# Kernel tuning notes

Measured on AMD Instinct MI355X. Metric: run time of the kernel, lower is better.

## Reference

```python
import jax, jax.numpy as jnp
import numpy as np

TEMP = 50.0  # softmax temperature from __init__ (temp=50.0)

N_SAMPLES = 32768
NUM_CANDIDATES = 2048
NUM_DIMS = 16


def setup_inputs() -> dict:
    key = jax.random.key(0)
    k1, k2, k3 = jax.random.split(key, 3)
    X = jax.random.normal(k1, (N_SAMPLES, NUM_DIMS), dtype=jnp.float32)
    Y = jax.random.normal(k2, (1, NUM_CANDIDATES, NUM_DIMS), dtype=jnp.float32)  # Y_rest param
    b = jax.random.normal(k3, (1, NUM_CANDIDATES), dtype=jnp.float32) * 0.1     # intercept_rest param
    return {"X": X, "Y": Y, "b": b}


def reference(X, Y, b):
    """FiniteModel.forward in convex mode with soft selection.

    scores[n, c] = <X[n], Y[0, c]> - b[0, c]           (dot-product kernel)
    weights      = softmax(temp * scores, axis=1)       (moded_max, soft mode)
    f_x[n]       = sum_c weights[n, c] * scores[n, c]
    choice[n, :] = sum_c weights[n, c] * Y[0, c, :]
    Returns (choice, f_x) as in the torch forward.
    """
    Yc = Y[0]                                     # [C, D]
    scores = jnp.einsum('nd,cd->nc', X, Yc) - b   # [N, C] (b broadcasts from [1, C])
    weights = jax.nn.softmax(TEMP * scores, axis=1)
    f_x = jnp.sum(weights * scores, axis=1)       # [N]
    choice = jnp.einsum('nc,cd->nd', weights, Yc) # [N, D]
    return choice, f_x
```

## Files before the change

kernel.cpp:

```cpp
#include <hip/hip_runtime.h>
#include <math.h>

#if defined(__has_builtin)
#  if __has_builtin(__builtin_amdgcn_exp2f)
#    define EXP2F(x) __builtin_amdgcn_exp2f(x)
#  else
#    define EXP2F(x) exp2f(x)
#  endif
#else
#  define EXP2F(x) exp2f(x)
#endif

constexpr int   DD = 16;
constexpr float T2 = 72.13475204444817f;
constexpr float DEFER_THR = 8.0f;

typedef __attribute__((ext_vector_type(8)))  short s16x8;
typedef __attribute__((ext_vector_type(16))) float f32x16;

static __device__ __forceinline__ s16x8 mk8(unsigned a, unsigned b, unsigned c, unsigned d) {
    union { unsigned u[4]; s16x8 v; } x;
    x.u[0] = a; x.u[1] = b; x.u[2] = c; x.u[3] = d;
    return x.v;
}
static __device__ __forceinline__ unsigned pack_tr(float a, float b) {
    return (__float_as_uint(a) >> 16) | (__float_as_uint(b) & 0xFFFF0000u);
}
static __device__ __forceinline__ float trunc_bf(float a) {
    return __uint_as_float(__float_as_uint(a) & 0xFFFF0000u);
}
static __device__ __forceinline__ unsigned short rne16(float f) {
    unsigned u = __float_as_uint(f);
    return (unsigned short)((u + 0x7FFFu + ((u >> 16) & 1u)) >> 16);
}
static __device__ __forceinline__ float bfh2f(unsigned short h) {
    return __uint_as_float(((unsigned)h) << 16);
}

__global__ void prep_kernel(const float* __restrict__ Y, const float* __restrict__ B,
                            unsigned short* __restrict__ YhA, unsigned short* __restrict__ YlA,
                            unsigned short* __restrict__ V3h, unsigned short* __restrict__ V3l,
                            unsigned* __restrict__ Bq, int C)
{
    int c = blockIdx.x * blockDim.x + threadIdx.x;
    if (c >= C) return;

    union { unsigned short u[DD]; s16x8 v[2]; } hb, lb;
    const float* yr = Y + (size_t)c * DD;
#pragma unroll
    for (int d = 0; d < DD; ++d) {
        float y = yr[d];
        unsigned short h = rne16(y);
        hb.u[d] = h;
        lb.u[d] = rne16(y - bfh2f(h));
    }
    s16x8* yh = (s16x8*)(YhA + (size_t)c * DD);
    s16x8* yl = (s16x8*)(YlA + (size_t)c * DD);
    yh[0] = hb.v[0]; yh[1] = hb.v[1];
    yl[0] = lb.v[0]; yl[1] = lb.v[1];

    float bb = B[c];
    float qb = -T2 * bb;
    unsigned short qh = rne16(qb);
    Bq[c] = (unsigned)qh | ((unsigned)rne16(qb - bfh2f(qh)) << 16);

    const int t = c >> 5, r = c & 31;
    union { unsigned short u[32]; s16x8 v[4]; } vh, vl;
#pragma unroll
    for (int slot = 0; slot < 32; ++slot) {
        int j = slot & 7, hs = (slot >> 3) & 1;
        int cl = (slot & 16) | (j & 3) | (hs << 2) | (((j >> 2) & 1) << 3);
        int cc = (t << 5) | cl;
        float v;
        if (r < DD)            v = Y[(size_t)cc * DD + r];
        else if (r == DD)      v = B[cc];
        else if (r == DD + 1)  v = 1.0f;
        else                   v = 0.0f;
        unsigned short h = rne16(v);
        vh.u[slot] = h;
        vl.u[slot] = rne16(v - bfh2f(h));
    }
    s16x8* ph = (s16x8*)(V3h + ((size_t)t * 32 + r) * 32);
    s16x8* pl = (s16x8*)(V3l + ((size_t)t * 32 + r) * 32);
#pragma unroll
    for (int q = 0; q < 4; ++q) { ph[q] = vh.v[q]; pl[q] = vl.v[q]; }
}

struct Frag {
    s16x8 aYh, aYl, vh0, vh1, vl0, vl1;
    unsigned bw;
};

__global__ __launch_bounds__(256, 4)
void finite_mfma(const float* __restrict__ X,
                 const unsigned short* __restrict__ YhA, const unsigned short* __restrict__ YlA,
                 const unsigned short* __restrict__ V3h, const unsigned short* __restrict__ V3l,
                 const unsigned* __restrict__ Bq,
                 float* __restrict__ out, int N, int C)
{
    const int tid  = threadIdx.x;
    const int wave = tid >> 6, lane = tid & 63;
    const int s = lane & 31, hi = lane >> 5;
    const int n0 = blockIdx.x * 32;
    const int cpw = C >> 2, cbase = wave * cpw, ntile = cpw >> 5;

    __shared__ float bufc[4][18][32];
    __shared__ float lds_m[4][32];

    const unsigned short* pYh = YhA + ((size_t)(cbase + s) * DD + 8 * hi);
    const unsigned short* pYl = YlA + ((size_t)(cbase + s) * DD + 8 * hi);
    const unsigned short* pVh = V3h + (((size_t)(cbase >> 5) * 32 + s) * 32 + 8 * hi);
    const unsigned short* pVl = V3l + (((size_t)(cbase >> 5) * 32 + s) * 32 + 8 * hi);
    const unsigned*       pBq = Bq + cbase + s;

    const float* xp = X + ((size_t)(n0 + s) * DD + 8 * hi);
    float xq[8];
#pragma unroll
    for (int jj = 0; jj < 8; ++jj) xq[jj] = xp[jj] * T2;
    unsigned xhw[4], xlw[4];
#pragma unroll
    for (int jj = 0; jj < 4; ++jj) {
        float a = xq[2 * jj], b = xq[2 * jj + 1];
        xhw[jj] = pack_tr(a, b);
        xlw[jj] = pack_tr(a - trunc_bf(a), b - trunc_bf(b));
    }
    const s16x8 xqh = mk8(xhw[0], xhw[1], xhw[2], xhw[3]);
    const s16x8 xql = mk8(xlw[0], xlw[1], xlw[2], xlw[3]);
    const s16x8 ones2 = mk8(hi ? 0u : 0x3F803F80u, 0u, 0u, 0u);

    f32x16 acc;
#pragma unroll
    for (int r = 0; r < 16; ++r) acc[r] = 0.0f;
    float m2 = -INFINITY;

#define LDF(F, k) do {                                              \
        (F).aYh = *(const s16x8*)(pYh + (size_t)(k) * 512);         \
        (F).aYl = *(const s16x8*)(pYl + (size_t)(k) * 512);         \
        (F).vh0 = *(const s16x8*)(pVh + (size_t)(k) * 1024);        \
        (F).vh1 = *(const s16x8*)(pVh + (size_t)(k) * 1024 + 16);   \
        (F).vl0 = *(const s16x8*)(pVl + (size_t)(k) * 1024);        \
        (F).vl1 = *(const s16x8*)(pVl + (size_t)(k) * 1024 + 16);   \
        (F).bw  = pBq[(size_t)(k) * 32];                            \
    } while (0)

#define PROC(F) do {                                                            \
        const s16x8 a2 = mk8(hi ? 0u : (F).bw, 0u, 0u, 0u);                     \
        f32x16 S;                                                               \
        _Pragma("unroll")                                                       \
        for (int r = 0; r < 16; ++r) S[r] = 0.0f;                               \
        S = __builtin_amdgcn_mfma_f32_32x32x16_bf16(a2,     ones2, S, 0, 0, 0); \
        S = __builtin_amdgcn_mfma_f32_32x32x16_bf16((F).aYh, xqh,  S, 0, 0, 0); \
        S = __builtin_amdgcn_mfma_f32_32x32x16_bf16((F).aYh, xql,  S, 0, 0, 0); \
        S = __builtin_amdgcn_mfma_f32_32x32x16_bf16((F).aYl, xqh,  S, 0, 0, 0); \
        float tm[8];                                                            \
        _Pragma("unroll")                                                       \
        for (int jj = 0; jj < 8; ++jj) tm[jj] = fmaxf(S[2 * jj], S[2 * jj + 1]);\
        _Pragma("unroll")                                                       \
        for (int jj = 0; jj < 4; ++jj) tm[jj] = fmaxf(tm[jj], tm[jj + 4]);      \
        tm[0] = fmaxf(fmaxf(tm[0], tm[2]), fmaxf(tm[1], tm[3]));                \
        float tmax = fmaxf(tm[0], __shfl_xor(tm[0], 32, 64));                   \
        if (__any(tmax > m2 + DEFER_THR)) {                                     \
            float nm = fmaxf(m2, tmax);                                         \
            float sc = EXP2F(m2 - nm);                                          \
            _Pragma("unroll")                                                   \
            for (int r = 0; r < 16; ++r) acc[r] *= sc;                          \
            m2 = nm;                                                            \
        }                                                                       \
        unsigned phw[8];                                                        \
        _Pragma("unroll")                                                       \
        for (int jj = 0; jj < 8; ++jj) {                                        \
            float e0 = EXP2F(S[2 * jj] - m2);                                   \
            float e1 = EXP2F(S[2 * jj + 1] - m2);                               \
            phw[jj] = pack_tr(e0, e1);                                          \
        }                                                                       \
        const s16x8 Bph0 = mk8(phw[0], phw[1], phw[2], phw[3]);                 \
        const s16x8 Bph1 = mk8(phw[4], phw[5], phw[6], phw[7]);                 \
        acc = __builtin_amdgcn_mfma_f32_32x32x16_bf16((F).vh0, Bph0, acc, 0, 0, 0); \
        acc = __builtin_amdgcn_mfma_f32_32x32x16_bf16((F).vl0, Bph0, acc, 0, 0, 0); \
        acc = __builtin_amdgcn_mfma_f32_32x32x16_bf16((F).vh1, Bph1, acc, 0, 0, 0); \
        acc = __builtin_amdgcn_mfma_f32_32x32x16_bf16((F).vl1, Bph1, acc, 0, 0, 0); \
    } while (0)

    Frag f0, f1;
    LDF(f0, 0);
    for (int t = 0; t < ntile; t += 2) {
        LDF(f1, t + 1);
        PROC(f0);
        if (t + 2 < ntile) LDF(f0, t + 2);
        PROC(f1);
    }
#undef LDF
#undef PROC

    if (hi == 0) lds_m[wave][s] = m2;
    __syncthreads();
    float mstar = fmaxf(fmaxf(lds_m[0][s], lds_m[1][s]), fmaxf(lds_m[2][s], lds_m[3][s]));
    float sw = EXP2F(m2 - mstar);
#pragma unroll
    for (int r = 0; r < 8; ++r) {
        int dv = (r & 3) + 8 * (r >> 2) + 4 * hi;
        bufc[wave][dv][s] = acc[r] * sw;
    }
    if (hi == 0) {
        bufc[wave][16][s] = acc[8] * sw;
        bufc[wave][17][s] = acc[9] * sw;
    }
    __syncthreads();

#pragma unroll
    for (int q = 0; q < 3; ++q) {
        int u = tid + 256 * q;
        if (u < 18 * 32) {
            int dv = u >> 5, ss = u & 31;
            bufc[0][dv][ss] = bufc[0][dv][ss] + bufc[1][dv][ss]
                            + bufc[2][dv][ss] + bufc[3][dv][ss];
        }
    }
    __syncthreads();

    {
        int ss = tid >> 3, d0 = (tid & 7) * 2;
        float inv = 1.0f / bufc[0][17][ss];
        float2 o = make_float2(bufc[0][d0][ss] * inv, bufc[0][d0 + 1][ss] * inv);
        *(float2*)(out + (size_t)(n0 + ss) * DD + d0) = o;
    }
    if (tid < 32) {
        float inv = 1.0f / bufc[0][17][tid];
        const float* xr = X + (size_t)(n0 + tid) * DD;
        float dot = 0.0f;
#pragma unroll
        for (int d = 0; d < DD; ++d) dot = fmaf(xr[d], bufc[0][d][tid], dot);
        out[(size_t)N * DD + n0 + tid] = (dot - bufc[0][16][tid]) * inv;
    }
}

extern "C" void kernel_launch(void* const* d_in, const int* in_sizes, int n_in,
                              void* d_out, int out_size, void* d_ws, size_t ws_size,
                              hipStream_t stream) {
    const float* X = (const float*)d_in[0];
    const float* Y = (const float*)d_in[1];
    const float* B = (const float*)d_in[2];
    float*     out = (float*)d_out;

    const int N = in_sizes[0] / DD;
    const int C = in_sizes[2];

    char* w = (char*)d_ws;
    unsigned short* YhA = (unsigned short*)(w);
    unsigned short* YlA = (unsigned short*)(w + (size_t)C * DD * 2);
    unsigned short* V3h = (unsigned short*)(w + (size_t)C * DD * 4);
    unsigned short* V3l = (unsigned short*)(w + (size_t)C * DD * 4 + (size_t)32 * C * 2);
    unsigned*       Bq  = (unsigned*)   (w + (size_t)C * DD * 4 + (size_t)32 * C * 4);

    hipLaunchKernelGGL(prep_kernel, dim3((C + 255) / 256), dim3(256), 0, stream,
                       Y, B, YhA, YlA, V3h, V3l, Bq, C);
    hipLaunchKernelGGL(finite_mfma, dim3(N / 32), dim3(256), 0, stream,
                       X, YhA, YlA, V3h, V3l, Bq, out, N, C);
}
```

Baseline: 86.74 us.

## Drop low-bf16 V operand, widen blocks to eight waves, parallelize prep

Removes the low-order bf16 split of the value matrix, which halves the accumulation MFMAs and the V loads per tile. Raises the block size to 512 threads so eight waves split the candidates, with wider LDS reduction buffers to match. The prep kernel now gives each V element its own thread instead of looping 32 slots per candidate. Dropping the low split lowers the precision of the weighted sums of Y and b, and the accumulation now relies on single-bf16 values.

```diff
diff --git a/kernel.cpp b/kernel.cpp
--- a/kernel.cpp
+++ b/kernel.cpp
@@ -39,78 +39,66 @@
 
 __global__ void prep_kernel(const float* __restrict__ Y, const float* __restrict__ B,
                             unsigned short* __restrict__ YhA, unsigned short* __restrict__ YlA,
-                            unsigned short* __restrict__ V3h, unsigned short* __restrict__ V3l,
-                            unsigned* __restrict__ Bq, int C)
+                            unsigned short* __restrict__ V3h, unsigned* __restrict__ Bq, int C)
 {
-    int c = blockIdx.x * blockDim.x + threadIdx.x;
-    if (c >= C) return;
-
-    union { unsigned short u[DD]; s16x8 v[2]; } hb, lb;
-    const float* yr = Y + (size_t)c * DD;
-#pragma unroll
-    for (int d = 0; d < DD; ++d) {
-        float y = yr[d];
-        unsigned short h = rne16(y);
-        hb.u[d] = h;
-        lb.u[d] = rne16(y - bfh2f(h));
-    }
-    s16x8* yh = (s16x8*)(YhA + (size_t)c * DD);
-    s16x8* yl = (s16x8*)(YlA + (size_t)c * DD);
-    yh[0] = hb.v[0]; yh[1] = hb.v[1];
-    yl[0] = lb.v[0]; yl[1] = lb.v[1];
-
-    float bb = B[c];
-    float qb = -T2 * bb;
-    unsigned short qh = rne16(qb);
-    Bq[c] = (unsigned)qh | ((unsigned)rne16(qb - bfh2f(qh)) << 16);
-
-    const int t = c >> 5, r = c & 31;
-    union { unsigned short u[32]; s16x8 v[4]; } vh, vl;
-#pragma unroll
-    for (int slot = 0; slot < 32; ++slot) {
+    int gid = blockIdx.x * blockDim.x + threadIdx.x;
+    if (gid < C) {
+        const int c = gid;
+        union { unsigned short u[DD]; s16x8 v[2]; } hb, lb;
+        const float* yr = Y + (size_t)c * DD;
+#pragma unroll
+        for (int d = 0; d < DD; ++d) {
+            float y = yr[d];
+            unsigned short h = rne16(y);
+            hb.u[d] = h;
+            lb.u[d] = rne16(y - bfh2f(h));
+        }
+        s16x8* yh = (s16x8*)(YhA + (size_t)c * DD);
+        s16x8* yl = (s16x8*)(YlA + (size_t)c * DD);
+        yh[0] = hb.v[0]; yh[1] = hb.v[1];
+        yl[0] = lb.v[0]; yl[1] = lb.v[1];
+
+        float qb = -T2 * B[c];
+        unsigned short qh = rne16(qb);
+        Bq[c] = (unsigned)qh | ((unsigned)rne16(qb - bfh2f(qh)) << 16);
+    } else if (gid < C + 32 * C) {
+        const int e = gid - C;
+        const int t = e >> 10, r = (e >> 5) & 31, slot = e & 31;
         int j = slot & 7, hs = (slot >> 3) & 1;
         int cl = (slot & 16) | (j & 3) | (hs << 2) | (((j >> 2) & 1) << 3);
         int cc = (t << 5) | cl;
         float v;
-        if (r < DD)            v = Y[(size_t)cc * DD + r];
-        else if (r == DD)      v = B[cc];
-        else if (r == DD + 1)  v = 1.0f;
-        else                   v = 0.0f;
-        unsigned short h = rne16(v);
-        vh.u[slot] = h;
-        vl.u[slot] = rne16(v - bfh2f(h));
-    }
-    s16x8* ph = (s16x8*)(V3h + ((size_t)t * 32 + r) * 32);
-    s16x8* pl = (s16x8*)(V3l + ((size_t)t * 32 + r) * 32);
-#pragma unroll
-    for (int q = 0; q < 4; ++q) { ph[q] = vh.v[q]; pl[q] = vl.v[q]; }
+        if (r < DD)           v = Y[(size_t)cc * DD + r];
+        else if (r == DD)     v = B[cc];
+        else if (r == DD + 1) v = 1.0f;
+        else                  v = 0.0f;
+        V3h[((size_t)t * 32 + r) * 32 + slot] = rne16(v);
+    }
 }
 
 struct Frag {
-    s16x8 aYh, aYl, vh0, vh1, vl0, vl1;
+    s16x8 aYh, aYl, vh0, vh1;
     unsigned bw;
 };
 
-__global__ __launch_bounds__(256, 4)
+__global__ __launch_bounds__(512, 8)
 void finite_mfma(const float* __restrict__ X,
                  const unsigned short* __restrict__ YhA, const unsigned short* __restrict__ YlA,
-                 const unsigned short* __restrict__ V3h, const unsigned short* __restrict__ V3l,
-                 const unsigned* __restrict__ Bq,
+                 const unsigned short* __restrict__ V3h, const unsigned* __restrict__ Bq,
                  float* __restrict__ out, int N, int C)
 {
     const int tid  = threadIdx.x;
     const int wave = tid >> 6, lane = tid & 63;
     const int s = lane & 31, hi = lane >> 5;
     const int n0 = blockIdx.x * 32;
-    const int cpw = C >> 2, cbase = wave * cpw, ntile = cpw >> 5;
-
-    __shared__ float bufc[4][18][32];
-    __shared__ float lds_m[4][32];
+    const int cpw = C >> 3, cbase = wave * cpw, ntile = cpw >> 5;
+
+    __shared__ float bufc[8][18][32];
+    __shared__ float lds_m[8][32];
 
     const unsigned short* pYh = YhA + ((size_t)(cbase + s) * DD + 8 * hi);
     const unsigned short* pYl = YlA + ((size_t)(cbase + s) * DD + 8 * hi);
     const unsigned short* pVh = V3h + (((size_t)(cbase >> 5) * 32 + s) * 32 + 8 * hi);
-    const unsigned short* pVl = V3l + (((size_t)(cbase >> 5) * 32 + s) * 32 + 8 * hi);
     const unsigned*       pBq = Bq + cbase + s;
 
     const float* xp = X + ((size_t)(n0 + s) * DD + 8 * hi);
@@ -138,8 +126,6 @@
         (F).aYl = *(const s16x8*)(pYl + (size_t)(k) * 512);         \
         (F).vh0 = *(const s16x8*)(pVh + (size_t)(k) * 1024);        \
         (F).vh1 = *(const s16x8*)(pVh + (size_t)(k) * 1024 + 16);   \
-        (F).vl0 = *(const s16x8*)(pVl + (size_t)(k) * 1024);        \
-        (F).vl1 = *(const s16x8*)(pVl + (size_t)(k) * 1024 + 16);   \
         (F).bw  = pBq[(size_t)(k) * 32];                            \
     } while (0)
 
@@ -176,9 +162,7 @@
         const s16x8 Bph0 = mk8(phw[0], phw[1], phw[2], phw[3]);                 \
         const s16x8 Bph1 = mk8(phw[4], phw[5], phw[6], phw[7]);                 \
         acc = __builtin_amdgcn_mfma_f32_32x32x16_bf16((F).vh0, Bph0, acc, 0, 0, 0); \
-        acc = __builtin_amdgcn_mfma_f32_32x32x16_bf16((F).vl0, Bph0, acc, 0, 0, 0); \
         acc = __builtin_amdgcn_mfma_f32_32x32x16_bf16((F).vh1, Bph1, acc, 0, 0, 0); \
-        acc = __builtin_amdgcn_mfma_f32_32x32x16_bf16((F).vl1, Bph1, acc, 0, 0, 0); \
     } while (0)
 
     Frag f0, f1;
@@ -194,7 +178,9 @@
 
     if (hi == 0) lds_m[wave][s] = m2;
     __syncthreads();
-    float mstar = fmaxf(fmaxf(lds_m[0][s], lds_m[1][s]), fmaxf(lds_m[2][s], lds_m[3][s]));
+    float mstar = lds_m[0][s];
+#pragma unroll
+    for (int w = 1; w < 8; ++w) mstar = fmaxf(mstar, lds_m[w][s]);
     float sw = EXP2F(m2 - mstar);
 #pragma unroll
     for (int r = 0; r < 8; ++r) {
@@ -208,21 +194,22 @@
     __syncthreads();
 
 #pragma unroll
-    for (int q = 0; q < 3; ++q) {
-        int u = tid + 256 * q;
+    for (int q = 0; q < 2; ++q) {
+        int u = tid + 512 * q;
         if (u < 18 * 32) {
             int dv = u >> 5, ss = u & 31;
-            bufc[0][dv][ss] = bufc[0][dv][ss] + bufc[1][dv][ss]
-                            + bufc[2][dv][ss] + bufc[3][dv][ss];
+            float sum = bufc[0][dv][ss];
+#pragma unroll
+            for (int w = 1; w < 8; ++w) sum += bufc[w][dv][ss];
+            bufc[0][dv][ss] = sum;
         }
     }
     __syncthreads();
 
     {
-        int ss = tid >> 3, d0 = (tid & 7) * 2;
+        int ss = tid >> 4, d0 = tid & 15;
         float inv = 1.0f / bufc[0][17][ss];
-        float2 o = make_float2(bufc[0][d0][ss] * inv, bufc[0][d0 + 1][ss] * inv);
-        *(float2*)(out + (size_t)(n0 + ss) * DD + d0) = o;
+        out[(size_t)(n0 + ss) * DD + d0] = bufc[0][d0][ss] * inv;
     }
     if (tid < 32) {
         float inv = 1.0f / bufc[0][17][tid];
@@ -249,11 +236,11 @@
     unsigned short* YhA = (unsigned short*)(w);
     unsigned short* YlA = (unsigned short*)(w + (size_t)C * DD * 2);
     unsigned short* V3h = (unsigned short*)(w + (size_t)C * DD * 4);
-    unsigned short* V3l = (unsigned short*)(w + (size_t)C * DD * 4 + (size_t)32 * C * 2);
-    unsigned*       Bq  = (unsigned*)   (w + (size_t)C * DD * 4 + (size_t)32 * C * 4);
-
-    hipLaunchKernelGGL(prep_kernel, dim3((C + 255) / 256), dim3(256), 0, stream,
-                       Y, B, YhA, YlA, V3h, V3l, Bq, C);
-    hipLaunchKernelGGL(finite_mfma, dim3(N / 32), dim3(256), 0, stream,
-                       X, YhA, YlA, V3h, V3l, Bq, out, N, C);
-}
+    unsigned*       Bq  = (unsigned*)   (w + (size_t)C * DD * 4 + (size_t)32 * C * 2);
+
+    const int prep_threads = C + 32 * C;
+    hipLaunchKernelGGL(prep_kernel, dim3((prep_threads + 255) / 256), dim3(256), 0, stream,
+                       Y, B, YhA, YlA, V3h, Bq, C);
+    hipLaunchKernelGGL(finite_mfma, dim3(N / 32), dim3(512), 0, stream,
+                       X, YhA, YlA, V3h, Bq, out, N, C);
+}
```

Result: slower. 181.6 us (+109.4%).
